# Kernel tuning notes

Measured on AMD Instinct MI355X. Metric: run time of the kernel, lower is better.

Reference implementation:

```python
import jax, jax.numpy as jnp
import numpy as np

HEADS = 20          # 1280 / 64 head_dim, standard SD UNet attention
LORA_SCALE = 1.0    # lora_scale init arg


def setup_inputs() -> dict:
    key = jax.random.key(0)
    ks = jax.random.split(key, 16)
    def w(k, shape, s=0.02):
        return jax.random.normal(k, shape, dtype=jnp.float32) * s
    H, C, R = 1280, 768, 64  # hidden_size, cross_attention_dim, lora_rank
    return {
        "hidden_states": jax.random.normal(ks[0], (16, 4096, H), dtype=jnp.float32),
        "encoder_hidden_states": jax.random.normal(ks[1], (16, 77, C), dtype=jnp.float32),
        # base attention projections (diffusers: q/k/v no bias, to_out has bias)
        "Wq": w(ks[2], (H, H)), "Wk": w(ks[3], (C, H)), "Wv": w(ks[4], (C, H)),
        "Wo": w(ks[5], (H, H)), "bo": jnp.zeros((H,), dtype=jnp.float32),
        # LoRA adapters (down: in->rank, up: rank->out, no bias)
        "q_down": w(ks[6], (H, R)), "q_up": w(ks[7], (R, H)),
        "k_down": w(ks[8], (C, R)), "k_up": w(ks[9], (R, H)),
        "v_down": w(ks[10], (C, R)), "v_up": w(ks[11], (R, H)),
        "o_down": w(ks[12], (H, R)), "o_up": w(ks[13], (R, H)),
    }


def reference(hidden_states, encoder_hidden_states, Wq, Wk, Wv, Wo, bo,
              q_down, q_up, k_down, k_up, v_down, v_up, o_down, o_up):
    b, sq, _ = hidden_states.shape
    # base projections + LoRA low-rank corrections
    q = hidden_states @ Wq + LORA_SCALE * ((hidden_states @ q_down) @ q_up)
    k = encoder_hidden_states @ Wk + LORA_SCALE * ((encoder_hidden_states @ k_down) @ k_up)
    v = encoder_hidden_states @ Wv + LORA_SCALE * ((encoder_hidden_states @ v_down) @ v_up)

    d = q.shape[-1] // HEADS
    def split_heads(x):  # [b, s, h*d] -> [b, h, s, d]
        return x.reshape(x.shape[0], x.shape[1], HEADS, d).transpose(0, 2, 1, 3)
    qh, kh, vh = split_heads(q), split_heads(k), split_heads(v)

    # scaled dot-product attention (no mask, non-causal, dropout=0)
    scale = 1.0 / np.sqrt(d).astype(np.float32)
    scores = jnp.einsum('bhqd,bhkd->bhqk', qh, kh) * scale
    probs = jax.nn.softmax(scores, axis=-1)
    attn_out = jnp.einsum('bhqk,bhkd->bhqd', probs, vh)
    attn_out = attn_out.transpose(0, 2, 1, 3).reshape(b, sq, HEADS * d)

    # output projection + LoRA on W_O
    out = attn_out @ Wo + bo + LORA_SCALE * ((attn_out @ o_down) @ o_up)
    return out
```

## Files before the change

kernel.cpp:

```cpp
#include <hip/hip_runtime.h>
#include <hip/hip_bf16.h>
#include <stdint.h>

typedef unsigned short u16;
typedef __attribute__((ext_vector_type(8))) short short8;
typedef __attribute__((ext_vector_type(4))) float f32x4;

__device__ __forceinline__ u16 f2bf(float f) {
  union { float f; unsigned u; } v; v.f = f;
  unsigned r = v.u + 0x7fffu + ((v.u >> 16) & 1u);
  return (u16)(r >> 16);
}

__device__ __forceinline__ unsigned pkbf2(float lo, float hi) {
  __hip_bfloat162 h2 = __float22bfloat162_rn(make_float2(lo, hi));
  unsigned u;
  __builtin_memcpy(&u, &h2, sizeof(u));
  return u;
}

__device__ __forceinline__ void g2lds16(const u16* g, u16* l) {
  __builtin_amdgcn_global_load_lds(
      (const __attribute__((address_space(1))) uint32_t*)g,
      (__attribute__((address_space(3))) uint32_t*)l, 16, 0, 0);
}

#define BAR()   asm volatile("s_barrier" ::: "memory")
#define LGKM0() asm volatile("s_waitcnt lgkmcnt(0)" ::: "memory")
#define VM8()   asm volatile("s_waitcnt vmcnt(8)" ::: "memory")
#define VM0()   asm volatile("s_waitcnt vmcnt(0)" ::: "memory")
#define PRIO1() __builtin_amdgcn_s_setprio(1)
#define PRIO0() __builtin_amdgcn_s_setprio(0)

#define QSCALE 0.18033688f

__global__ __launch_bounds__(256) void k_convert_pad(const float* __restrict__ in,
                                                     u16* __restrict__ out,
                                                     int n8_valid, int n8_total) {
  int i = blockIdx.x * 256 + threadIdx.x;
  if (i >= n8_total) return;
  short8 o;
  if (i < n8_valid) {
    const float4* p = (const float4*)(in + (size_t)i * 8);
    float4 a = p[0], b = p[1];
    o[0] = (short)f2bf(a.x); o[1] = (short)f2bf(a.y);
    o[2] = (short)f2bf(a.z); o[3] = (short)f2bf(a.w);
    o[4] = (short)f2bf(b.x); o[5] = (short)f2bf(b.y);
    o[6] = (short)f2bf(b.z); o[7] = (short)f2bf(b.w);
  } else {
#pragma unroll
    for (int e = 0; e < 8; ++e) o[e] = 0;
  }
  *(short8*)(out + (size_t)i * 8) = o;
}

__global__ __launch_bounds__(256) void k_fusew(const float* __restrict__ W,
                                               const float* __restrict__ dn_g,
                                               const float* __restrict__ up_g,
                                               u16* __restrict__ Wt, int K, int N) {
  __shared__ float dn[64][65];
  __shared__ float up[64][17];
  const int k0 = blockIdx.x * 64, n0 = blockIdx.y * 16;
  const int kc = threadIdx.x & 63, ty = threadIdx.x >> 6;
  for (int c = threadIdx.x; c < 4096; c += 256)
    dn[c >> 6][c & 63] = dn_g[(size_t)(k0 + (c >> 6)) * 64 + (c & 63)];
  for (int c = threadIdx.x; c < 1024; c += 256)
    up[c >> 4][c & 15] = up_g[(size_t)(c >> 4) * N + n0 + (c & 15)];
  __syncthreads();
  float acc[4];
#pragma unroll
  for (int e = 0; e < 4; ++e)
    acc[e] = W[(size_t)(k0 + kc) * N + n0 + ty * 4 + e];
#pragma unroll 16
  for (int r = 0; r < 64; ++r) {
    float d = dn[kc][r];
#pragma unroll
    for (int e = 0; e < 4; ++e) acc[e] += d * up[r][ty * 4 + e];
  }
#pragma unroll
  for (int e = 0; e < 4; ++e)
    Wt[(size_t)(n0 + ty * 4 + e) * K + k0 + kc] = f2bf(acc[e]);
}

template <int OUT_MODE>
__global__ __launch_bounds__(256) void k_gemm(const u16* __restrict__ A,
                                              const u16* __restrict__ Bt,
                                              void* __restrict__ Cout,
                                              const float* __restrict__ bias,
                                              int M, int N, int K) {
  __shared__ __align__(16) u16 As[128 * 32];
  __shared__ __align__(16) u16 Bs[128 * 32];
  const int tid = threadIdx.x, lane = tid & 63, w = tid >> 6;
  const int n0 = blockIdx.x * 128, m0 = blockIdx.y * 128;
  const int wm = (w >> 1) * 64, wn = (w & 1) * 64;

  f32x4 acc[4][4];
  f32x4 zf = {0.f, 0.f, 0.f, 0.f};
#pragma unroll
  for (int i = 0; i < 4; ++i)
#pragma unroll
    for (int j = 0; j < 4; ++j) acc[i][j] = zf;

  const int c0 = w, c1 = w + 4;
  const int rA0 = c0 * 16 + (lane >> 2), rA1 = c1 * 16 + (lane >> 2);
  const int kp = (lane & 3) * 8;
  const u16* gA0 = A + (size_t)(m0 + rA0) * K + kp;
  const u16* gA1 = A + (size_t)(m0 + rA1) * K + kp;
  const u16* gB0 = Bt + (size_t)(n0 + rA0) * K + kp;
  const u16* gB1 = Bt + (size_t)(n0 + rA1) * K + kp;
  u16* lA0 = As + c0 * 512;  u16* lA1 = As + c1 * 512;
  u16* lB0 = Bs + c0 * 512;  u16* lB1 = Bs + c1 * 512;

  const int fr = lane & 15, kg = (lane >> 4) * 8;

  for (int k0 = 0; k0 < K; k0 += 32) {
    g2lds16(gA0 + k0, lA0);
    g2lds16(gA1 + k0, lA1);
    g2lds16(gB0 + k0, lB0);
    g2lds16(gB1 + k0, lB1);
    __syncthreads();
    short8 af[4], bf[4];
#pragma unroll
    for (int i = 0; i < 4; ++i)
      af[i] = *(const short8*)(As + (wm + i * 16 + fr) * 32 + kg);
#pragma unroll
    for (int j = 0; j < 4; ++j)
      bf[j] = *(const short8*)(Bs + (wn + j * 16 + fr) * 32 + kg);
#pragma unroll
    for (int i = 0; i < 4; ++i)
#pragma unroll
      for (int j = 0; j < 4; ++j)
        acc[i][j] = __builtin_amdgcn_mfma_f32_16x16x32_bf16(af[i], bf[j], acc[i][j], 0, 0, 0);
    __syncthreads();
  }

  const int rb = (lane >> 4) * 4;
  if (OUT_MODE == 0) {
    u16* C = (u16*)Cout;
#pragma unroll
    for (int i = 0; i < 4; ++i)
#pragma unroll
      for (int j = 0; j < 4; ++j) {
        int col = n0 + wn + j * 16 + fr;
#pragma unroll
        for (int r = 0; r < 4; ++r) {
          int row = m0 + wm + i * 16 + rb + r;
          C[(size_t)row * N + col] = f2bf(acc[i][j][r]);
        }
      }
  } else {
    float* C = (float*)Cout;
#pragma unroll
    for (int i = 0; i < 4; ++i)
#pragma unroll
      for (int j = 0; j < 4; ++j) {
        int col = n0 + wn + j * 16 + fr;
        float bj = bias[col];
#pragma unroll
        for (int r = 0; r < 4; ++r) {
          int row = m0 + wm + i * 16 + rb + r;
          C[(size_t)row * N + col] = acc[i][j][r] + bj;
        }
      }
  }
}


#define GEMM256_TILE_RD()                                                      \
  constexpr int K = 1280;                                                      \
  constexpr int N = 1280;                                                      \
  __shared__ __align__(16) u16 lds[2][2][2][128 * 64];                         \
  const int lane = threadIdx.x & 63, w = threadIdx.x >> 6;                     \
  const int bid = blockIdx.x;                                                  \
  const int tile = (bid & 7) * 160 + (bid >> 3);                               \
  const int n0 = (tile % 5) * 256, m0 = (tile / 5) * 256;                      \
  const int l0 = w * 2;                                                        \
  const int fr = lane & 15;                                                    \
  const int q16b = (lane >> 4) * 16;                                           \
  const int xr = (fr & 7) << 4;                                                \
  const int cT0 = ((0 + q16b) ^ xr) >> 1;                                      \
  const int cT1 = ((64 + q16b) ^ xr) >> 1;                                     \
  const int ha = w >> 2;                                                       \
  const int hb = (w & 3) >> 1;                                                 \
  const int rB0 = (w & 1) * 64;

#define LOAD_AF(P, IB)                                                         \
  do {                                                                         \
    _Pragma("unroll") for (int ii = 0; ii < 4; ++ii) {                         \
      const u16* rp = &lds[P][0][ha][(((IB) + ii) * 16 + fr) * 64];            \
      af[ii][0] = *(const short8*)(rp + cT0);                                  \
      af[ii][1] = *(const short8*)(rp + cT1);                                  \
    }                                                                          \
  } while (0)

#define LOAD_BF(P, JB)                                                         \
  do {                                                                         \
    _Pragma("unroll") for (int jj = 0; jj < 2; ++jj) {                         \
      const u16* rp = &lds[P][1][hb][(rB0 + ((JB) + jj) * 16 + fr) * 64];      \
      bf[(JB) + jj][0] = *(const short8*)(rp + cT0);                           \
      bf[(JB) + jj][1] = *(const short8*)(rp + cT1);                           \
    }                                                                          \
  } while (0)

#define MFMA_Q(IO, JB)                                                         \
  do {                                                                         \
    _Pragma("unroll") for (int t = 0; t < 2; ++t)                              \
        _Pragma("unroll") for (int ii = 0; ii < 4; ++ii)                       \
            _Pragma("unroll") for (int jj = 0; jj < 2; ++jj)                   \
                acc[(IO) + ii][(JB) + jj] =                                    \
        __builtin_amdgcn_mfma_f32_16x16x32_bf16(                               \
            af[ii][t], bf[(JB) + jj][t], acc[(IO) + ii][(JB) + jj], 0, 0, 0);  \
  } while (0)

#define ACC_ZERO()                                                             \
  do {                                                                         \
    f32x4 zf = {0.f, 0.f, 0.f, 0.f};                                           \
    _Pragma("unroll") for (int i = 0; i < 8; ++i)                              \
        _Pragma("unroll") for (int j = 0; j < 4; ++j) acc[i][j] = zf;          \
  } while (0)

template <int OUT_MODE>
__global__ __launch_bounds__(512, 2) void k_gemm256f(const u16* __restrict__ A,
                                                     const u16* __restrict__ Bt,
                                                     void* __restrict__ Cout,
                                                     const float* __restrict__ bias) {
  GEMM256_TILE_RD();
  const u16* gsrc[8];
#pragma unroll
  for (int s = 0; s < 8; ++s) {
    const int side = s >> 2, h = (s >> 1) & 1, l = s & 1;
    const int o = (l0 + l) * 1024 + lane * 16;
    const int row = o >> 7;
    const int scol = (o & 127) ^ ((row & 7) << 4);
    const u16* base = side ? (Bt + (size_t)(n0 + h * 128 + row) * K)
                           : (A + (size_t)(m0 + h * 128 + row) * K);
    gsrc[s] = base + (scol >> 1);
  }

#define STAGE(P, KT)                                                           \
  do {                                                                         \
    _Pragma("unroll") for (int s = 0; s < 8; ++s) {                            \
      const int side = s >> 2, h = (s >> 1) & 1, l = s & 1;                    \
      g2lds16(gsrc[s] + (KT) * 64, &lds[P][side][h][(l0 + l) * 512]);          \
    }                                                                          \
  } while (0)

  short8 af[4][2], bf[4][2];
  f32x4 acc[8][4];
  ACC_ZERO();

  STAGE(0, 0);
  STAGE(1, 1);
  VM8();
  BAR();

  for (int t = 0; t < 20; ++t) {
    const int P = t & 1;
    LOAD_AF(P, 0);
    LOAD_BF(P, 0);
    LOAD_BF(P, 2);
    MFMA_Q(0, 0);
    MFMA_Q(0, 2);
    LOAD_AF(P, 4);
    MFMA_Q(4, 2);
    LGKM0();
    BAR();
    if (t < 18) STAGE(P, t + 2);
    PRIO1(); MFMA_Q(4, 0); PRIO0();
    if (t < 18) { VM8(); } else { VM0(); }
    BAR();
  }
#undef STAGE

  const int rb = (lane >> 4) * 4;
  const int orow = m0 + (w >> 2) * 128;
  const int ocol = n0 + (w & 3) * 64;
  if (OUT_MODE == 0) {
    u16* C = (u16*)Cout;
#pragma unroll
    for (int i = 0; i < 8; ++i)
#pragma unroll
      for (int j = 0; j < 4; ++j) {
        const int col = ocol + j * 16 + fr;
#pragma unroll
        for (int r = 0; r < 4; ++r)
          C[(size_t)(orow + i * 16 + rb + r) * N + col] = f2bf(acc[i][j][r]);
      }
  } else {
    float* C = (float*)Cout;
#pragma unroll
    for (int i = 0; i < 8; ++i)
#pragma unroll
      for (int j = 0; j < 4; ++j) {
        const int col = ocol + j * 16 + fr;
        const float bj = bias[col];
#pragma unroll
        for (int r = 0; r < 4; ++r)
          C[(size_t)(orow + i * 16 + rb + r) * N + col] = acc[i][j][r] + bj;
      }
  }
}

__global__ __launch_bounds__(512, 2) void k_gemm256q(const float* __restrict__ A,
                                                     const u16* __restrict__ Bt,
                                                     u16* __restrict__ Cout) {
  GEMM256_TILE_RD();
  const u16* gB[4];
#pragma unroll
  for (int s = 0; s < 4; ++s) {
    const int h = s >> 1, l = s & 1;
    const int o = (l0 + l) * 1024 + lane * 16;
    const int row = o >> 7;
    const int scol = (o & 127) ^ ((row & 7) << 4);
    gB[s] = Bt + (size_t)(n0 + h * 128 + row) * K + (scol >> 1);
  }
  const float* gA[4];
  int aoff[4];
#pragma unroll
  for (int s = 0; s < 4; ++s) {
    const int h = s >> 1, l = s & 1;
    const int o = (l0 + l) * 1024 + lane * 16;
    const int row = o >> 7;
    gA[s] = A + (size_t)(m0 + h * 128 + row) * K + ((o & 127) >> 1);
    aoff[s] = row * 64 + (((o & 127) ^ ((row & 7) << 4)) >> 1);
  }

#define ALOADQ(KT)                                                             \
  do {                                                                         \
    _Pragma("unroll") for (int s = 0; s < 4; ++s) {                            \
      const float4* p_ = (const float4*)(gA[s] + (KT) * 64);                   \
      av[s][0] = p_[0];                                                        \
      av[s][1] = p_[1];                                                        \
    }                                                                          \
  } while (0)

#define ASTOREQ(P)                                                             \
  do {                                                                         \
    _Pragma("unroll") for (int s = 0; s < 4; ++s) {                            \
      uint4 pk_;                                                               \
      pk_.x = pkbf2(av[s][0].x, av[s][0].y);                                   \
      pk_.y = pkbf2(av[s][0].z, av[s][0].w);                                   \
      pk_.z = pkbf2(av[s][1].x, av[s][1].y);                                   \
      pk_.w = pkbf2(av[s][1].z, av[s][1].w);                                   \
      *(uint4*)(&lds[(P)][0][s >> 1][aoff[s]]) = pk_;                          \
    }                                                                          \
  } while (0)

#define BSTAGEQ(P, KT)                                                         \
  do {                                                                         \
    _Pragma("unroll") for (int s = 0; s < 4; ++s)                              \
      g2lds16(gB[s] + (KT) * 64, &lds[(P)][1][s >> 1][(l0 + (s & 1)) * 512]);  \
  } while (0)

  short8 af[4][2], bf[4][2];
  f32x4 acc[8][4];
  float4 av[4][2];
  ACC_ZERO();

  ALOADQ(0); ASTOREQ(0); BSTAGEQ(0, 0);
  ALOADQ(1); ASTOREQ(1); BSTAGEQ(1, 1);
  ALOADQ(2);
  VM0();
  LGKM0();
  BAR();

  for (int t = 0; t < 20; ++t) {
    const int P = t & 1;
    LOAD_AF(P, 0);
    LOAD_BF(P, 0);
    LOAD_BF(P, 2);
    MFMA_Q(0, 0);
    MFMA_Q(0, 2);
    LOAD_AF(P, 4);
    MFMA_Q(4, 2);
    LGKM0();
    BAR();
    if (t < 18) {
      VM0();
      ASTOREQ(P);
      BSTAGEQ(P, t + 2);
      if (t < 17) ALOADQ(t + 3);
    } else if (t == 18) {
      VM0();
    }
    PRIO1(); MFMA_Q(4, 0); PRIO0();
    LGKM0();
    BAR();
  }
#undef ALOADQ
#undef ASTOREQ
#undef BSTAGEQ

  const int rb = (lane >> 4) * 4;
  const int orow = m0 + (w >> 2) * 128;
  const int ocol = n0 + (w & 3) * 64;
#pragma unroll
  for (int i = 0; i < 8; ++i)
#pragma unroll
    for (int j = 0; j < 4; ++j) {
      const int col = ocol + j * 16 + fr;
#pragma unroll
      for (int r = 0; r < 4; ++r)
        Cout[(size_t)(orow + i * 16 + rb + r) * N + col] = f2bf(acc[i][j][r] * QSCALE);
    }
}

__global__ __launch_bounds__(256) void k_attn(u16* __restrict__ Q,
                                              const u16* __restrict__ Kb,
                                              const u16* __restrict__ Vb) {
  const int mt = blockIdx.x, h = blockIdx.y, b = blockIdx.z;
  const int tid = threadIdx.x, lane = tid & 63, w = tid >> 6;
  const int m0 = b * 4096 + mt * 128;
  const int ccol = h * 64;

  __shared__ __align__(16) u16 Kl[80 * 72];
  __shared__ __align__(16) u16 Vt[64 * 104];
  __shared__ __align__(16) u16 Pl[128 * 104];

  {
    short8 z;
#pragma unroll
    for (int e = 0; e < 8; ++e) z[e] = 0;
    for (int i = tid; i < 720; i += 256)  ((short8*)Kl)[i] = z;
    for (int i = tid; i < 832; i += 256)  ((short8*)Vt)[i] = z;
    for (int i = tid; i < 1664; i += 256) ((short8*)Pl)[i] = z;
  }
  __syncthreads();

  for (int c = tid; c < 616; c += 256) {
    int s = c >> 3, d0 = (c & 7) * 8;
    short8 v = *(const short8*)(Kb + (size_t)(b * 77 + s) * 1280 + ccol + d0);
    *(short8*)(Kl + s * 72 + d0) = v;
  }
  for (int c = tid; c < 616; c += 256) {
    int s = c >> 3, d0 = (c & 7) * 8;
    short8 v = *(const short8*)(Vb + (size_t)(b * 77 + s) * 1280 + ccol + d0);
#pragma unroll
    for (int e = 0; e < 8; ++e) Vt[(d0 + e) * 104 + s] = (u16)v[e];
  }

  const int cb = lane & 15, kg = (lane >> 4) * 8;
  short8 qf[2][2];
#pragma unroll
  for (int i = 0; i < 2; ++i)
#pragma unroll
    for (int t = 0; t < 2; ++t) {
      int row = m0 + w * 32 + i * 16 + cb;
      qf[i][t] = *(const short8*)(Q + (size_t)row * 1280 + ccol + t * 32 + kg);
    }
  __syncthreads();

  f32x4 sc[2][5];
  {
    f32x4 zf = {0.f, 0.f, 0.f, 0.f};
#pragma unroll
    for (int i = 0; i < 2; ++i)
#pragma unroll
      for (int j = 0; j < 5; ++j) sc[i][j] = zf;
  }
#pragma unroll
  for (int t = 0; t < 2; ++t) {
    short8 kf[5];
#pragma unroll
    for (int j = 0; j < 5; ++j)
      kf[j] = *(const short8*)(Kl + (j * 16 + cb) * 72 + t * 32 + kg);
#pragma unroll
    for (int i = 0; i < 2; ++i)
#pragma unroll
      for (int j = 0; j < 5; ++j)
        sc[i][j] = __builtin_amdgcn_mfma_f32_16x16x32_bf16(qf[i][t], kf[j], sc[i][j], 0, 0, 0);
  }

  float inv[2][4];
#pragma unroll
  for (int i = 0; i < 2; ++i) {
#pragma unroll
    for (int r = 0; r < 4; ++r) {
      float sum = 0.f;
#pragma unroll
      for (int j = 0; j < 4; ++j) {
        float pv = exp2f(sc[i][j][r]);
        sc[i][j][r] = pv;
        sum += pv;
      }
      {
        float pv = (cb < 13) ? exp2f(sc[i][4][r]) : 0.f;
        sc[i][4][r] = pv;
        sum += pv;
      }
#pragma unroll
      for (int mk = 8; mk >= 1; mk >>= 1) sum += __shfl_xor(sum, mk, 64);
      inv[i][r] = 1.f / sum;
    }
  }

  {
    int rbase = (lane >> 4) * 4;
#pragma unroll
    for (int i = 0; i < 2; ++i)
#pragma unroll
      for (int j = 0; j < 5; ++j)
#pragma unroll
        for (int r = 0; r < 4; ++r)
          Pl[(w * 32 + i * 16 + rbase + r) * 104 + j * 16 + cb] = f2bf(sc[i][j][r]);
  }
  __syncthreads();

  f32x4 o[2][4];
  {
    f32x4 zf = {0.f, 0.f, 0.f, 0.f};
#pragma unroll
    for (int i = 0; i < 2; ++i)
#pragma unroll
      for (int n = 0; n < 4; ++n) o[i][n] = zf;
  }
#pragma unroll
  for (int t = 0; t < 3; ++t) {
    short8 pf[2], vf[4];
#pragma unroll
    for (int i = 0; i < 2; ++i)
      pf[i] = *(const short8*)(Pl + (w * 32 + i * 16 + cb) * 104 + t * 32 + kg);
#pragma unroll
    for (int n = 0; n < 4; ++n)
      vf[n] = *(const short8*)(Vt + (n * 16 + cb) * 104 + t * 32 + kg);
#pragma unroll
    for (int i = 0; i < 2; ++i)
#pragma unroll
      for (int n = 0; n < 4; ++n)
        o[i][n] = __builtin_amdgcn_mfma_f32_16x16x32_bf16(pf[i], vf[n], o[i][n], 0, 0, 0);
  }

  {
    int rbase = (lane >> 4) * 4;
#pragma unroll
    for (int i = 0; i < 2; ++i)
#pragma unroll
      for (int n = 0; n < 4; ++n)
#pragma unroll
        for (int r = 0; r < 4; ++r) {
          int row = m0 + w * 32 + i * 16 + rbase + r;
          Q[(size_t)row * 1280 + ccol + n * 16 + cb] = f2bf(o[i][n][r] * inv[i][r]);
        }
  }
}

extern "C" void kernel_launch(void* const* d_in, const int* in_sizes, int n_in,
                              void* d_out, int out_size, void* d_ws, size_t ws_size,
                              hipStream_t stream) {
  (void)in_sizes; (void)n_in; (void)out_size; (void)ws_size;
  const float* hs  = (const float*)d_in[0];
  const float* ehs = (const float*)d_in[1];
  const float* Wq  = (const float*)d_in[2];
  const float* Wk  = (const float*)d_in[3];
  const float* Wv  = (const float*)d_in[4];
  const float* Wo  = (const float*)d_in[5];
  const float* bo  = (const float*)d_in[6];
  const float* qd  = (const float*)d_in[7];
  const float* qu  = (const float*)d_in[8];
  const float* kd  = (const float*)d_in[9];
  const float* ku  = (const float*)d_in[10];
  const float* vd  = (const float*)d_in[11];
  const float* vu  = (const float*)d_in[12];
  const float* od  = (const float*)d_in[13];
  const float* ou  = (const float*)d_in[14];

  char* p = (char*)d_ws;
  u16* q_buf = (u16*)p;  p += (size_t)65536 * 1280 * 2;
  u16* wq_t  = (u16*)p;  p += (size_t)1280 * 1280 * 2;
  u16* wo_t  = (u16*)p;  p += (size_t)1280 * 1280 * 2;
  u16* wk_t  = (u16*)p;  p += (size_t)1280 * 768 * 2;
  u16* wv_t  = (u16*)p;  p += (size_t)1280 * 768 * 2;
  u16* ehs_b = (u16*)p;  p += (size_t)1280 * 768 * 2;
  u16* k_buf = (u16*)p;  p += (size_t)1280 * 1280 * 2;
  u16* v_buf = (u16*)p;  p += (size_t)1280 * 1280 * 2;

  k_convert_pad<<<480, 256, 0, stream>>>(ehs, ehs_b, 118272, 122880);

  k_fusew<<<dim3(20, 80), 256, 0, stream>>>(Wq, qd, qu, wq_t, 1280, 1280);
  k_fusew<<<dim3(12, 80), 256, 0, stream>>>(Wk, kd, ku, wk_t, 768, 1280);
  k_fusew<<<dim3(12, 80), 256, 0, stream>>>(Wv, vd, vu, wv_t, 768, 1280);
  k_fusew<<<dim3(20, 80), 256, 0, stream>>>(Wo, od, ou, wo_t, 1280, 1280);

  k_gemm256q<<<1280, 512, 0, stream>>>(hs, wq_t, q_buf);
  k_gemm<0><<<dim3(10, 10), 256, 0, stream>>>(ehs_b, wk_t, k_buf, nullptr, 1280, 1280, 768);
  k_gemm<0><<<dim3(10, 10), 256, 0, stream>>>(ehs_b, wv_t, v_buf, nullptr, 1280, 1280, 768);

  k_attn<<<dim3(32, 20, 16), 256, 0, stream>>>(q_buf, k_buf, v_buf);

  k_gemm256f<1><<<1280, 512, 0, stream>>>(q_buf, wo_t, d_out, bo);
}
```

Measured before the change: 755.3 us.

## Pre-convert hidden states to bf16 and enlarge attention tiles to 256 rows

Adds a separate conversion pass that turns the fp32 hidden states into bf16, staged in the output buffer. The Q projection then uses the generic bf16 GEMM with a new scaled-bf16 output mode, replacing the dedicated kernel that converted fp32 A tiles on the fly. The attention kernel now runs 512 threads over 256 query rows per block and zeroes only the padding regions of LDS instead of whole buffers. The trade is a full extra read and write of the 84M-element activation in exchange for a simpler, async-staged GEMM main loop, plus fewer and larger attention blocks.

```diff
diff --git a/kernel.cpp b/kernel.cpp
--- a/kernel.cpp
+++ b/kernel.cpp
@@ -10,13 +10,6 @@
   union { float f; unsigned u; } v; v.f = f;
   unsigned r = v.u + 0x7fffu + ((v.u >> 16) & 1u);
   return (u16)(r >> 16);
-}
-
-__device__ __forceinline__ unsigned pkbf2(float lo, float hi) {
-  __hip_bfloat162 h2 = __float22bfloat162_rn(make_float2(lo, hi));
-  unsigned u;
-  __builtin_memcpy(&u, &h2, sizeof(u));
-  return u;
 }
 
 __device__ __forceinline__ void g2lds16(const u16* g, u16* l) {
@@ -33,6 +26,20 @@
 #define PRIO0() __builtin_amdgcn_s_setprio(0)
 
 #define QSCALE 0.18033688f
+
+__global__ __launch_bounds__(256) void k_convert(const float* __restrict__ in,
+                                                 u16* __restrict__ out, int n8) {
+  int i = blockIdx.x * 256 + threadIdx.x;
+  if (i >= n8) return;
+  const float4* p = (const float4*)(in + (size_t)i * 8);
+  float4 a = p[0], b = p[1];
+  short8 o;
+  o[0] = (short)f2bf(a.x); o[1] = (short)f2bf(a.y);
+  o[2] = (short)f2bf(a.z); o[3] = (short)f2bf(a.w);
+  o[4] = (short)f2bf(b.x); o[5] = (short)f2bf(b.y);
+  o[6] = (short)f2bf(b.z); o[7] = (short)f2bf(b.w);
+  *(short8*)(out + (size_t)i * 8) = o;
+}
 
 __global__ __launch_bounds__(256) void k_convert_pad(const float* __restrict__ in,
                                                      u16* __restrict__ out,
@@ -286,7 +293,7 @@
         for (int r = 0; r < 4; ++r)
           C[(size_t)(orow + i * 16 + rb + r) * N + col] = f2bf(acc[i][j][r]);
       }
-  } else {
+  } else if (OUT_MODE == 1) {
     float* C = (float*)Cout;
 #pragma unroll
     for (int i = 0; i < 8; ++i)
@@ -298,141 +305,52 @@
         for (int r = 0; r < 4; ++r)
           C[(size_t)(orow + i * 16 + rb + r) * N + col] = acc[i][j][r] + bj;
       }
-  }
-}
-
-__global__ __launch_bounds__(512, 2) void k_gemm256q(const float* __restrict__ A,
-                                                     const u16* __restrict__ Bt,
-                                                     u16* __restrict__ Cout) {
-  GEMM256_TILE_RD();
-  const u16* gB[4];
-#pragma unroll
-  for (int s = 0; s < 4; ++s) {
-    const int h = s >> 1, l = s & 1;
-    const int o = (l0 + l) * 1024 + lane * 16;
-    const int row = o >> 7;
-    const int scol = (o & 127) ^ ((row & 7) << 4);
-    gB[s] = Bt + (size_t)(n0 + h * 128 + row) * K + (scol >> 1);
-  }
-  const float* gA[4];
-  int aoff[4];
-#pragma unroll
-  for (int s = 0; s < 4; ++s) {
-    const int h = s >> 1, l = s & 1;
-    const int o = (l0 + l) * 1024 + lane * 16;
-    const int row = o >> 7;
-    gA[s] = A + (size_t)(m0 + h * 128 + row) * K + ((o & 127) >> 1);
-    aoff[s] = row * 64 + (((o & 127) ^ ((row & 7) << 4)) >> 1);
-  }
-
-#define ALOADQ(KT)                                                             \
-  do {                                                                         \
-    _Pragma("unroll") for (int s = 0; s < 4; ++s) {                            \
-      const float4* p_ = (const float4*)(gA[s] + (KT) * 64);                   \
-      av[s][0] = p_[0];                                                        \
-      av[s][1] = p_[1];                                                        \
-    }                                                                          \
-  } while (0)
-
-#define ASTOREQ(P)                                                             \
-  do {                                                                         \
-    _Pragma("unroll") for (int s = 0; s < 4; ++s) {                            \
-      uint4 pk_;                                                               \
-      pk_.x = pkbf2(av[s][0].x, av[s][0].y);                                   \
-      pk_.y = pkbf2(av[s][0].z, av[s][0].w);                                   \
-      pk_.z = pkbf2(av[s][1].x, av[s][1].y);                                   \
-      pk_.w = pkbf2(av[s][1].z, av[s][1].w);                                   \
-      *(uint4*)(&lds[(P)][0][s >> 1][aoff[s]]) = pk_;                          \
-    }                                                                          \
-  } while (0)
-
-#define BSTAGEQ(P, KT)                                                         \
-  do {                                                                         \
-    _Pragma("unroll") for (int s = 0; s < 4; ++s)                              \
-      g2lds16(gB[s] + (KT) * 64, &lds[(P)][1][s >> 1][(l0 + (s & 1)) * 512]);  \
-  } while (0)
-
-  short8 af[4][2], bf[4][2];
-  f32x4 acc[8][4];
-  float4 av[4][2];
-  ACC_ZERO();
-
-  ALOADQ(0); ASTOREQ(0); BSTAGEQ(0, 0);
-  ALOADQ(1); ASTOREQ(1); BSTAGEQ(1, 1);
-  ALOADQ(2);
-  VM0();
-  LGKM0();
-  BAR();
-
-  for (int t = 0; t < 20; ++t) {
-    const int P = t & 1;
-    LOAD_AF(P, 0);
-    LOAD_BF(P, 0);
-    LOAD_BF(P, 2);
-    MFMA_Q(0, 0);
-    MFMA_Q(0, 2);
-    LOAD_AF(P, 4);
-    MFMA_Q(4, 2);
-    LGKM0();
-    BAR();
-    if (t < 18) {
-      VM0();
-      ASTOREQ(P);
-      BSTAGEQ(P, t + 2);
-      if (t < 17) ALOADQ(t + 3);
-    } else if (t == 18) {
-      VM0();
-    }
-    PRIO1(); MFMA_Q(4, 0); PRIO0();
-    LGKM0();
-    BAR();
-  }
-#undef ALOADQ
-#undef ASTOREQ
-#undef BSTAGEQ
-
-  const int rb = (lane >> 4) * 4;
-  const int orow = m0 + (w >> 2) * 128;
-  const int ocol = n0 + (w & 3) * 64;
-#pragma unroll
-  for (int i = 0; i < 8; ++i)
-#pragma unroll
-    for (int j = 0; j < 4; ++j) {
-      const int col = ocol + j * 16 + fr;
-#pragma unroll
-      for (int r = 0; r < 4; ++r)
-        Cout[(size_t)(orow + i * 16 + rb + r) * N + col] = f2bf(acc[i][j][r] * QSCALE);
-    }
-}
-
-__global__ __launch_bounds__(256) void k_attn(u16* __restrict__ Q,
+  } else {
+    u16* C = (u16*)Cout;
+#pragma unroll
+    for (int i = 0; i < 8; ++i)
+#pragma unroll
+      for (int j = 0; j < 4; ++j) {
+        const int col = ocol + j * 16 + fr;
+#pragma unroll
+        for (int r = 0; r < 4; ++r)
+          C[(size_t)(orow + i * 16 + rb + r) * N + col] = f2bf(acc[i][j][r] * QSCALE);
+      }
+  }
+}
+
+__global__ __launch_bounds__(512) void k_attn(u16* __restrict__ Q,
                                               const u16* __restrict__ Kb,
                                               const u16* __restrict__ Vb) {
   const int mt = blockIdx.x, h = blockIdx.y, b = blockIdx.z;
   const int tid = threadIdx.x, lane = tid & 63, w = tid >> 6;
-  const int m0 = b * 4096 + mt * 128;
+  const int m0 = b * 4096 + mt * 256;
   const int ccol = h * 64;
 
   __shared__ __align__(16) u16 Kl[80 * 72];
   __shared__ __align__(16) u16 Vt[64 * 104];
-  __shared__ __align__(16) u16 Pl[128 * 104];
+  __shared__ __align__(16) u16 Pl[256 * 104];
 
   {
     short8 z;
 #pragma unroll
     for (int e = 0; e < 8; ++e) z[e] = 0;
-    for (int i = tid; i < 720; i += 256)  ((short8*)Kl)[i] = z;
-    for (int i = tid; i < 832; i += 256)  ((short8*)Vt)[i] = z;
-    for (int i = tid; i < 1664; i += 256) ((short8*)Pl)[i] = z;
+    if (tid < 27) ((short8*)Kl)[693 + tid] = z;
+    {
+      int row = tid >> 1, c0 = 80 + (tid & 1) * 8;
+      *(short8*)(Pl + row * 104 + c0) = z;
+    }
+    for (int c = tid; c < 2048; c += 512)
+      Vt[(c >> 5) * 104 + 64 + (c & 31)] = 0;
   }
   __syncthreads();
 
-  for (int c = tid; c < 616; c += 256) {
+  for (int c = tid; c < 616; c += 512) {
     int s = c >> 3, d0 = (c & 7) * 8;
     short8 v = *(const short8*)(Kb + (size_t)(b * 77 + s) * 1280 + ccol + d0);
     *(short8*)(Kl + s * 72 + d0) = v;
   }
-  for (int c = tid; c < 616; c += 256) {
+  for (int c = tid; c < 616; c += 512) {
     int s = c >> 3, d0 = (c & 7) * 8;
     short8 v = *(const short8*)(Vb + (size_t)(b * 77 + s) * 1280 + ccol + d0);
 #pragma unroll
@@ -573,7 +491,9 @@
   u16* ehs_b = (u16*)p;  p += (size_t)1280 * 768 * 2;
   u16* k_buf = (u16*)p;  p += (size_t)1280 * 1280 * 2;
   u16* v_buf = (u16*)p;  p += (size_t)1280 * 1280 * 2;
-
+  u16* hs_b  = (u16*)d_out;
+
+  k_convert<<<40960, 256, 0, stream>>>(hs, hs_b, 10485760);
   k_convert_pad<<<480, 256, 0, stream>>>(ehs, ehs_b, 118272, 122880);
 
   k_fusew<<<dim3(20, 80), 256, 0, stream>>>(Wq, qd, qu, wq_t, 1280, 1280);
@@ -581,11 +501,11 @@
   k_fusew<<<dim3(12, 80), 256, 0, stream>>>(Wv, vd, vu, wv_t, 768, 1280);
   k_fusew<<<dim3(20, 80), 256, 0, stream>>>(Wo, od, ou, wo_t, 1280, 1280);
 
-  k_gemm256q<<<1280, 512, 0, stream>>>(hs, wq_t, q_buf);
+  k_gemm256f<2><<<1280, 512, 0, stream>>>(hs_b, wq_t, q_buf, nullptr);
   k_gemm<0><<<dim3(10, 10), 256, 0, stream>>>(ehs_b, wk_t, k_buf, nullptr, 1280, 1280, 768);
   k_gemm<0><<<dim3(10, 10), 256, 0, stream>>>(ehs_b, wv_t, v_buf, nullptr, 1280, 1280, 768);
 
-  k_attn<<<dim3(32, 20, 16), 256, 0, stream>>>(q_buf, k_buf, v_buf);
+  k_attn<<<dim3(16, 20, 16), 512, 0, stream>>>(q_buf, k_buf, v_buf);
 
   k_gemm256f<1><<<1280, 512, 0, stream>>>(q_buf, wo_t, d_out, bo);
 }
```

Result: slower. 783.9 us (+3.8%).
